# Performance work log

Hardware: AMD Instinct MI355X
Metric: run time of the kernel (lower is better)

Reference implementation:

```python
import jax, jax.numpy as jnp
import numpy as np

B, T, N, D = 8, 12, 325, 256
H = 8
HD = D // H
FF = 1024
SCALE = HD ** -0.5
EPS = 1e-5
NEG_INF = jnp.float32(-1e30)


def layernorm(x, w, b):
    mu = jnp.mean(x, axis=-1, keepdims=True)
    var = jnp.mean(jnp.square(x - mu), axis=-1, keepdims=True)
    return (x - mu) * jax.lax.rsqrt(var + EPS) * w + b


def mha(x, wq, bq, wk, bk, wv, bv, wo, bo, mask):
    # x: (G, L, D); mask: (L, L) bool, True = keep, or None
    G, L, _ = x.shape
    q = (x @ wq + bq).reshape(G, L, H, HD)
    k = (x @ wk + bk).reshape(G, L, H, HD)
    v = (x @ wv + bv).reshape(G, L, H, HD)
    scores = jnp.einsum('glhd,gmhd->ghlm', q, k) * SCALE
    if mask is not None:
        scores = jnp.where(mask[None, None], scores, NEG_INF)
    attn = jax.nn.softmax(scores, axis=-1)
    out = jnp.einsum('ghlm,gmhd->glhd', attn, v).reshape(G, L, D)
    return out @ wo + bo


def setup_inputs() -> dict:
    key = jax.random.key(0)
    ks = jax.random.split(key, 16)
    s = 0.02
    inp = {
        'x': jax.random.normal(ks[0], (B, T, N, D), jnp.float32),
        'adj_mask': jax.random.randint(ks[1], (N, N), 0, 2, jnp.int32),
        'sa_wq': jax.random.normal(ks[2], (D, D)) * s, 'sa_bq': jnp.zeros((D,)),
        'sa_wk': jax.random.normal(ks[3], (D, D)) * s, 'sa_bk': jnp.zeros((D,)),
        'sa_wv': jax.random.normal(ks[4], (D, D)) * s, 'sa_bv': jnp.zeros((D,)),
        'sa_wo': jax.random.normal(ks[5], (D, D)) * s, 'sa_bo': jnp.zeros((D,)),
        'sa_ln_w': jnp.ones((D,)), 'sa_ln_b': jnp.zeros((D,)),
        'ta_wq': jax.random.normal(ks[6], (D, D)) * s, 'ta_bq': jnp.zeros((D,)),
        'ta_wk': jax.random.normal(ks[7], (D, D)) * s, 'ta_bk': jnp.zeros((D,)),
        'ta_wv': jax.random.normal(ks[8], (D, D)) * s, 'ta_bv': jnp.zeros((D,)),
        'ta_wo': jax.random.normal(ks[9], (D, D)) * s, 'ta_bo': jnp.zeros((D,)),
        'ta_ln_w': jnp.ones((D,)), 'ta_ln_b': jnp.zeros((D,)),
        'f_w1': jax.random.normal(ks[10], (D, FF)) * s, 'f_b1': jnp.zeros((FF,)),
        'f_w2': jax.random.normal(ks[11], (FF, D)) * s, 'f_b2': jnp.zeros((D,)),
        'f_ln_w': jnp.ones((D,)), 'f_ln_b': jnp.zeros((D,)),
    }
    return inp


def reference(x, adj_mask,
              sa_wq, sa_bq, sa_wk, sa_bk, sa_wv, sa_bv, sa_wo, sa_bo, sa_ln_w, sa_ln_b,
              ta_wq, ta_bq, ta_wk, ta_bk, ta_wv, ta_bv, ta_wo, ta_bo, ta_ln_w, ta_ln_b,
              f_w1, f_b1, f_w2, f_b2, f_ln_w, f_ln_b):
    # Spatial attention over N at each (b, t)
    xs = x.reshape(B * T, N, D)
    sa = mha(xs, sa_wq, sa_bq, sa_wk, sa_bk, sa_wv, sa_bv, sa_wo, sa_bo,
             adj_mask != 0).reshape(B, T, N, D)
    x = layernorm(x + sa, sa_ln_w, sa_ln_b)

    # Temporal attention over T at each (b, n), causal
    xt = x.transpose(0, 2, 1, 3).reshape(B * N, T, D)
    causal = jnp.tril(jnp.ones((T, T), dtype=bool))
    ta = mha(xt, ta_wq, ta_bq, ta_wk, ta_bk, ta_wv, ta_bv, ta_wo, ta_bo, causal)
    ta = ta.reshape(B, N, T, D).transpose(0, 2, 1, 3)
    x = layernorm(x + ta, ta_ln_w, ta_ln_b)

    # FFN with exact GELU (torch nn.GELU default)
    h = jax.nn.gelu(x @ f_w1 + f_b1, approximate=False)
    out = layernorm(x + (h @ f_w2 + f_b2), f_ln_w, f_ln_b)
    return out
```

## Files before the change

kernel.cpp:

```cpp
#include <hip/hip_runtime.h>
#include <hip/hip_bf16.h>
#include <math.h>

#define B_   8
#define T_   12
#define NN   325
#define DD   256
#define HH   8
#define HD   32
#define FFD  1024
#define MTOK (B_*T_*NN)
#define QKVD 768
#define ATT_SCALE 0.17677669529663687f
#define LN_EPS 1e-5f
#define NEG_BIG (-1e30f)

typedef __attribute__((ext_vector_type(8))) __bf16 bf16x8;
typedef __attribute__((ext_vector_type(4))) float  f32x4;
typedef __attribute__((ext_vector_type(4))) short  shortx4;
typedef __attribute__((ext_vector_type(8))) unsigned short ushortx8;

static __device__ inline float bf2f(unsigned short u) {
  union { float f; unsigned int i; } c; c.i = ((unsigned int)u) << 16; return c.f;
}

#if __has_builtin(__builtin_amdgcn_mfma_f32_16x16x16bf16_1k)
#define MFMA16(a,b,c) __builtin_amdgcn_mfma_f32_16x16x16bf16_1k((a),(b),(c),0,0,0)
#else
static __device__ inline f32x4 mfma16_fn(shortx4 a, shortx4 b, f32x4 c) {
  f32x4 d;
  asm volatile("v_mfma_f32_16x16x16_bf16 %0, %1, %2, %3"
               : "=v"(d) : "v"(a), "v"(b), "v"(c));
  return d;
}
#define MFMA16(a,b,c) mfma16_fn((a),(b),(c))
#endif

#define GLDS(gsrc, ldst) \
  __builtin_amdgcn_global_load_lds((const __attribute__((address_space(1))) void*)(gsrc), \
                                   (__attribute__((address_space(3))) void*)(ldst), 16, 0, 0)

__global__ __launch_bounds__(256) void gemm_mfma(
    const __hip_bfloat16* __restrict__ A,
    const __hip_bfloat16* __restrict__ Wt,
    const float* __restrict__ bias,
    float* __restrict__ Cf, __hip_bfloat16* __restrict__ Cb,
    int Mr, int Nr, int Kr, int mode)
{
  __shared__ __hip_bfloat16 As[2][128 * 32];
  __shared__ __hip_bfloat16 Bs[2][128 * 32];

  const int NB  = Nr >> 7;
  const int nwg = gridDim.x;
  {
  }
  const int orig = blockIdx.x;
  const int qq = nwg >> 3, rr = nwg & 7;
  const int xcd = orig & 7, off = orig >> 3;
  const int id = (xcd < rr ? xcd * (qq + 1) : rr * (qq + 1) + (xcd - rr) * qq) + off;
  const int n0 = (id % NB) * 128;
  const int m0 = (id / NB) * 128;

  const int tid  = threadIdx.x;
  const int w    = tid >> 6;
  const int lane = tid & 63;
  const int wr   = w >> 1, wc = w & 1;

  f32x4 acc[4][4] = {};

  const int srow = w * 32 + (lane >> 2);
  const int scol = (lane & 3) * 8;
  int ar0 = m0 + srow;      if (ar0 >= Mr) ar0 = Mr - 1;
  int ar1 = m0 + srow + 16; if (ar1 >= Mr) ar1 = Mr - 1;
  const size_t aOff0 = (size_t)ar0 * Kr + scol;
  const size_t aOff1 = (size_t)ar1 * Kr + scol;
  const size_t bOff0 = (size_t)(n0 + srow) * Kr + scol;
  const size_t bOff1 = (size_t)(n0 + srow + 16) * Kr + scol;

  const int lr = lane & 15;
  const int kb = (lane >> 4) * 8;
  const int nk = Kr >> 5;

#define STAGE_T(buf, k0) do { \
    GLDS(&A[aOff0 + (k0)],  &As[buf][(w * 32) * 32]); \
    GLDS(&A[aOff1 + (k0)],  &As[buf][(w * 32 + 16) * 32]); \
    GLDS(&Wt[bOff0 + (k0)], &Bs[buf][(w * 32) * 32]); \
    GLDS(&Wt[bOff1 + (k0)], &Bs[buf][(w * 32 + 16) * 32]); \
  } while (0)

#define COMPUTE_T(buf) do { \
    bf16x8 af[4], bfr[4]; \
    _Pragma("unroll") for (int i = 0; i < 4; ++i) { \
      af[i]  = *(const bf16x8*)&As[buf][(wr * 64 + i * 16 + lr) * 32 + kb]; \
      bfr[i] = *(const bf16x8*)&Bs[buf][(wc * 64 + i * 16 + lr) * 32 + kb]; \
    } \
    _Pragma("unroll") for (int i = 0; i < 4; ++i) \
      _Pragma("unroll") for (int j = 0; j < 4; ++j) \
        acc[i][j] = __builtin_amdgcn_mfma_f32_16x16x32_bf16(af[i], bfr[j], acc[i][j], 0, 0, 0); \
  } while (0)

  STAGE_T(0, 0);
  __syncthreads();
  int cur = 0;
  for (int k = 1; k < nk; ++k) {
    STAGE_T(cur ^ 1, k * 32);
    COMPUTE_T(cur);
    __syncthreads();
    cur ^= 1;
  }
  COMPUTE_T(cur);
#undef STAGE_T
#undef COMPUTE_T

  const int rg = lane >> 4;
  #pragma unroll
  for (int i = 0; i < 4; ++i) {
    int rowb = m0 + wr * 64 + i * 16 + rg * 4;
    #pragma unroll
    for (int j = 0; j < 4; ++j) {
      int col = n0 + wc * 64 + j * 16 + lr;
      float bv = bias[col];
      #pragma unroll
      for (int q = 0; q < 4; ++q) {
        int gm = rowb + q;
        if (gm >= Mr) continue;
        float c = acc[i][j][q] + bv;
        if (mode == 0) {
          Cf[(size_t)gm * Nr + col] = c;
        } else {
          if (mode == 1) c = 0.5f * c * (1.f + erff(c * 0.70710678118654752f));
          Cb[(size_t)gm * Nr + col] = __float2bfloat16(c);
        }
      }
    }
  }
}

__global__ __launch_bounds__(256) void wt_cvt(
    const float* __restrict__ W, __hip_bfloat16* __restrict__ Wt, int K, int N)
{
  __shared__ float t[32][33];
  const int n0 = blockIdx.x * 32, k0 = blockIdx.y * 32;
  const int tx = threadIdx.x & 31, ty = threadIdx.x >> 5;
  #pragma unroll
  for (int i = 0; i < 32; i += 8)
    t[ty + i][tx] = W[(size_t)(k0 + ty + i) * N + n0 + tx];
  __syncthreads();
  #pragma unroll
  for (int i = 0; i < 32; i += 8)
    Wt[(size_t)(n0 + ty + i) * K + k0 + tx] = __float2bfloat16(t[tx][ty + i]);
}

__global__ __launch_bounds__(256) void cvt_bf16(
    const float* __restrict__ x, __hip_bfloat16* __restrict__ y, int n4)
{
  int i = blockIdx.x * 256 + threadIdx.x;
  if (i >= n4) return;
  float4 v = reinterpret_cast<const float4*>(x)[i];
  union { shortx4 s; __hip_bfloat16 h[4]; } u;
  u.h[0] = __float2bfloat16(v.x); u.h[1] = __float2bfloat16(v.y);
  u.h[2] = __float2bfloat16(v.z); u.h[3] = __float2bfloat16(v.w);
  reinterpret_cast<shortx4*>(y)[i] = u.s;
}

__global__ __launch_bounds__(256) void bias_cat3(
    const float* __restrict__ a, const float* __restrict__ b,
    const float* __restrict__ c, float* __restrict__ o)
{
  int i = blockIdx.x * 256 + threadIdx.x;
  if (i < 256) o[i] = a[i];
  else if (i < 512) o[i] = b[i - 256];
  else if (i < 768) o[i] = c[i - 512];
}

__global__ __launch_bounds__(256) void maskpack(
    const int* __restrict__ adj, unsigned int* __restrict__ mb)
{
  int idx = blockIdx.x * 256 + threadIdx.x;
  if (idx >= NN * 11) return;
  int l = idx / 11, w = idx % 11;
  unsigned int bits = 0;
  #pragma unroll 4
  for (int b = 0; b < 32; ++b) {
    int m = w * 32 + b;
    if (m < NN && adj[l * NN + m] != 0) bits |= (1u << b);
  }
  mb[idx] = bits;
}

__global__ __launch_bounds__(256) void spatial_attn_mfma(
    const __hip_bfloat16* __restrict__ qkv,
    const unsigned int* __restrict__ mb,
    __hip_bfloat16* __restrict__ out)
{
  constexpr int KP = 40;
  constexpr int VP = 340;
  __shared__ unsigned short Kl[336 * KP];
  __shared__ unsigned short Vt[32 * VP];

  const int g = blockIdx.x, h = blockIdx.y;
  const int tid = threadIdx.x;
  const int w = tid >> 6, lane = tid & 63;
  const int lq = lane & 15, lg = lane >> 4;

  const size_t baseQ = (size_t)g * NN * QKVD + (size_t)h * HD;
  const size_t baseK = baseQ + 256;
  const size_t baseV = baseQ + 512;

  for (int idx = tid; idx < 32 * (VP - NN); idx += 256) {
    int d = idx / (VP - NN), kk = NN + idx % (VP - NN);
    Vt[d * VP + kk] = 0;
  }
  for (int idx = tid; idx < NN * 4; idx += 256) {
    int row = idx >> 2, cc = (idx & 3) * 8;
    union { bf16x8 v; unsigned short u[8]; } kv, vv;
    kv.v = *(const bf16x8*)&qkv[baseK + (size_t)row * QKVD + cc];
    *(bf16x8*)&Kl[row * KP + cc] = kv.v;
    vv.v = *(const bf16x8*)&qkv[baseV + (size_t)row * QKVD + cc];
    #pragma unroll
    for (int j = 0; j < 8; ++j) Vt[(cc + j) * VP + row] = vv.u[j];
  }
  __syncthreads();

  for (int qt = w; qt < 21; qt += 4) {
    const int query = qt * 16 + lq;
    const int qc = query < NN ? query : NN - 1;
    const bf16x8 qf = *(const bf16x8*)&qkv[baseQ + (size_t)qc * QKVD + lg * 8];
    const unsigned int* mrow = &mb[qc * 11];

    f32x4 accL = {0.f, 0.f, 0.f, 0.f};
    f32x4 accH = {0.f, 0.f, 0.f, 0.f};
    float mrun = -INFINITY, lrun = 0.f;

    for (int t = 0; t < 21; ++t) {
      bf16x8 kf = *(const bf16x8*)&Kl[(t * 16 + lq) * KP + lg * 8];
      f32x4 st = __builtin_amdgcn_mfma_f32_16x16x32_bf16(
          kf, qf, (f32x4){0.f, 0.f, 0.f, 0.f}, 0, 0, 0);
      const unsigned int mw = mrow[t >> 1];
      const int kbase = t * 16 + lg * 4;
      const int bbase = (t & 1) * 16 + lg * 4;
      float s[4];
      #pragma unroll
      for (int q = 0; q < 4; ++q) {
        float fill = (kbase + q < NN) ? NEG_BIG : -INFINITY;
        s[q] = ((mw >> (bbase + q)) & 1u) ? st[q] * ATT_SCALE : fill;
      }
      float tmax = fmaxf(fmaxf(s[0], s[1]), fmaxf(s[2], s[3]));
      tmax = fmaxf(tmax, __shfl_xor(tmax, 16));
      tmax = fmaxf(tmax, __shfl_xor(tmax, 32));
      const float mnew = fmaxf(mrun, tmax);
      const float corr = __expf(mrun - mnew);
      float p0 = __expf(s[0] - mnew), p1 = __expf(s[1] - mnew);
      float p2 = __expf(s[2] - mnew), p3 = __expf(s[3] - mnew);
      float ps = p0 + p1 + p2 + p3;
      ps += __shfl_xor(ps, 16);
      ps += __shfl_xor(ps, 32);
      lrun = lrun * corr + ps;
      mrun = mnew;
      accL *= corr; accH *= corr;
      union { shortx4 s4; __hip_bfloat16 hh[4]; } up;
      up.hh[0] = __float2bfloat16(p0); up.hh[1] = __float2bfloat16(p1);
      up.hh[2] = __float2bfloat16(p2); up.hh[3] = __float2bfloat16(p3);
      shortx4 vaL = *(const shortx4*)&Vt[lq * VP + kbase];
      shortx4 vaH = *(const shortx4*)&Vt[(lq + 16) * VP + kbase];
      accL = MFMA16(vaL, up.s4, accL);
      accH = MFMA16(vaH, up.s4, accH);
    }

    if (query < NN) {
      const float inv = 1.f / lrun;
      const size_t ob = ((size_t)(g * NN + query)) * DD + (size_t)h * HD;
      union { shortx4 s4; __hip_bfloat16 hh[4]; } uL, uH;
      #pragma unroll
      for (int q = 0; q < 4; ++q) {
        uL.hh[q] = __float2bfloat16(accL[q] * inv);
        uH.hh[q] = __float2bfloat16(accH[q] * inv);
      }
      *(shortx4*)&out[ob + lg * 4]      = uL.s4;
      *(shortx4*)&out[ob + 16 + lg * 4] = uH.s4;
    }
  }
}

__global__ __launch_bounds__(256) void temporal_attn(
    const __hip_bfloat16* __restrict__ qkv, __hip_bfloat16* __restrict__ out)
{
  int idx = blockIdx.x * 256 + threadIdx.x;
  const int total = B_ * NN * HH * T_;
  if (idx >= total) return;

  int t  = idx % T_;
  int h  = (idx / T_) % HH;
  int n  = (idx / (T_ * HH)) % NN;
  int b  = idx / (T_ * HH * NN);

  const size_t tq = (size_t)((b * T_ + t) * NN + n) * QKVD + h * HD;
  float qr[HD];
  #pragma unroll
  for (int c8 = 0; c8 < 4; ++c8) {
    ushortx8 u = *(const ushortx8*)&qkv[tq + c8 * 8];
    #pragma unroll
    for (int j = 0; j < 8; ++j) qr[c8 * 8 + j] = bf2f(u[j]);
  }

  float o[HD] = {};
  float mrun = -INFINITY, lrun = 0.f;

  for (int tt = 0; tt <= t; ++tt) {
    const size_t tk = (size_t)((b * T_ + tt) * NN + n) * QKVD + h * HD;
    float s = 0.f;
    #pragma unroll
    for (int c8 = 0; c8 < 4; ++c8) {
      ushortx8 u = *(const ushortx8*)&qkv[tk + 256 + c8 * 8];
      #pragma unroll
      for (int j = 0; j < 8; ++j) s += qr[c8 * 8 + j] * bf2f(u[j]);
    }
    s *= ATT_SCALE;

    float mnew = fmaxf(mrun, s);
    float corr = __expf(mrun - mnew);
    float p = __expf(s - mnew);
    lrun = lrun * corr + p;
    #pragma unroll
    for (int c8 = 0; c8 < 4; ++c8) {
      ushortx8 u = *(const ushortx8*)&qkv[tk + 512 + c8 * 8];
      #pragma unroll
      for (int j = 0; j < 8; ++j) o[c8 * 8 + j] = o[c8 * 8 + j] * corr + p * bf2f(u[j]);
    }
    mrun = mnew;
  }

  float inv = 1.f / lrun;
  __hip_bfloat16* op = out + ((size_t)((b * T_ + t) * NN + n)) * DD + h * HD;
  #pragma unroll
  for (int d0 = 0; d0 < HD; d0 += 4) {
    union { shortx4 s; __hip_bfloat16 h4[4]; } u;
    #pragma unroll
    for (int j = 0; j < 4; ++j) u.h4[j] = __float2bfloat16(o[d0 + j] * inv);
    *reinterpret_cast<shortx4*>(op + d0) = u.s;
  }
}

__global__ __launch_bounds__(64) void add_ln(
    const float* __restrict__ x, const float* __restrict__ r,
    const float* __restrict__ w, const float* __restrict__ bb,
    float* __restrict__ y, __hip_bfloat16* __restrict__ ybf)
{
  const size_t row = blockIdx.x;
  const int lane = threadIdx.x;

  const float4 xv = reinterpret_cast<const float4*>(x + row * DD)[lane];
  const float4 rv = reinterpret_cast<const float4*>(r + row * DD)[lane];
  float e[4] = {xv.x + rv.x, xv.y + rv.y, xv.z + rv.z, xv.w + rv.w};

  float s  = e[0] + e[1] + e[2] + e[3];
  float ss = e[0]*e[0] + e[1]*e[1] + e[2]*e[2] + e[3]*e[3];
  #pragma unroll
  for (int off = 32; off > 0; off >>= 1) {
    s  += __shfl_xor(s,  off, 64);
    ss += __shfl_xor(ss, off, 64);
  }
  float mu  = s * (1.f / DD);
  float var = ss * (1.f / DD) - mu * mu;
  float rs  = rsqrtf(var + LN_EPS);

  const float4 wv = reinterpret_cast<const float4*>(w)[lane];
  const float4 bv = reinterpret_cast<const float4*>(bb)[lane];
  float o0 = (e[0] - mu) * rs * wv.x + bv.x;
  float o1 = (e[1] - mu) * rs * wv.y + bv.y;
  float o2 = (e[2] - mu) * rs * wv.z + bv.z;
  float o3 = (e[3] - mu) * rs * wv.w + bv.w;
  float4 yv = {o0, o1, o2, o3};
  reinterpret_cast<float4*>(y + row * DD)[lane] = yv;
  if (ybf) {
    union { shortx4 s4; __hip_bfloat16 h4[4]; } u;
    u.h4[0] = __float2bfloat16(o0); u.h4[1] = __float2bfloat16(o1);
    u.h4[2] = __float2bfloat16(o2); u.h4[3] = __float2bfloat16(o3);
    reinterpret_cast<shortx4*>(ybf + row * DD)[lane] = u.s4;
  }
}

extern "C" void kernel_launch(void* const* d_in, const int* in_sizes, int n_in,
                              void* d_out, int out_size, void* d_ws, size_t ws_size,
                              hipStream_t stream)
{
  const float* x0   = (const float*)d_in[0];
  const int*   adj  = (const int*)  d_in[1];
  const float* sa_wq = (const float*)d_in[2];
  const float* sa_bq = (const float*)d_in[3];
  const float* sa_wk = (const float*)d_in[4];
  const float* sa_bk = (const float*)d_in[5];
  const float* sa_wv = (const float*)d_in[6];
  const float* sa_bv = (const float*)d_in[7];
  const float* sa_wo = (const float*)d_in[8];
  const float* sa_bo = (const float*)d_in[9];
  const float* sa_lw = (const float*)d_in[10];
  const float* sa_lb = (const float*)d_in[11];
  const float* ta_wq = (const float*)d_in[12];
  const float* ta_bq = (const float*)d_in[13];
  const float* ta_wk = (const float*)d_in[14];
  const float* ta_bk = (const float*)d_in[15];
  const float* ta_wv = (const float*)d_in[16];
  const float* ta_bv = (const float*)d_in[17];
  const float* ta_wo = (const float*)d_in[18];
  const float* ta_bo = (const float*)d_in[19];
  const float* ta_lw = (const float*)d_in[20];
  const float* ta_lb = (const float*)d_in[21];
  const float* f_w1  = (const float*)d_in[22];
  const float* f_b1  = (const float*)d_in[23];
  const float* f_w2  = (const float*)d_in[24];
  const float* f_b2  = (const float*)d_in[25];
  const float* f_lw  = (const float*)d_in[26];
  const float* f_lb  = (const float*)d_in[27];

  float* out = (float*)d_out;
  float* ws  = (float*)d_ws;

  const size_t P = (size_t)MTOK * DD;
  if (ws_size < 7 * P * sizeof(float)) return;

  float* R0 = ws;
  __hip_bfloat16* QKVb = (__hip_bfloat16*)(ws + P);
  __hip_bfloat16* HIDb = (__hip_bfloat16*)(ws + P);
  float* R3 = ws + 3 * P;
  float* R4 = ws + 4 * P;
  __hip_bfloat16* X0b  = (__hip_bfloat16*)(ws + 5 * P);
  __hip_bfloat16* X1b  = (__hip_bfloat16*)(ws + 5 * P + P / 2);
  __hip_bfloat16* ATTb = (__hip_bfloat16*)(ws + 6 * P);
  __hip_bfloat16* Wb   = (__hip_bfloat16*)(ws + 6 * P + P / 2);

  __hip_bfloat16* sa_qkv_t = Wb;
  __hip_bfloat16* ta_qkv_t = Wb + 196608;
  __hip_bfloat16* sa_wo_t  = Wb + 393216;
  __hip_bfloat16* ta_wo_t  = Wb + 458752;
  __hip_bfloat16* f_w1_t   = Wb + 524288;
  __hip_bfloat16* f_w2_t   = Wb + 786432;
  float* sa_qkvb = (float*)(Wb + 1048576);
  float* ta_qkvb = sa_qkvb + 768;
  unsigned int* MB = (unsigned int*)(ta_qkvb + 768);

  wt_cvt<<<dim3(DD/32, DD/32), 256, 0, stream>>>(sa_wq, sa_qkv_t,          DD, DD);
  wt_cvt<<<dim3(DD/32, DD/32), 256, 0, stream>>>(sa_wk, sa_qkv_t + 65536,  DD, DD);
  wt_cvt<<<dim3(DD/32, DD/32), 256, 0, stream>>>(sa_wv, sa_qkv_t + 131072, DD, DD);
  wt_cvt<<<dim3(DD/32, DD/32), 256, 0, stream>>>(ta_wq, ta_qkv_t,          DD, DD);
  wt_cvt<<<dim3(DD/32, DD/32), 256, 0, stream>>>(ta_wk, ta_qkv_t + 65536,  DD, DD);
  wt_cvt<<<dim3(DD/32, DD/32), 256, 0, stream>>>(ta_wv, ta_qkv_t + 131072, DD, DD);
  wt_cvt<<<dim3(DD/32, DD/32), 256, 0, stream>>>(sa_wo, sa_wo_t, DD, DD);
  wt_cvt<<<dim3(DD/32, DD/32), 256, 0, stream>>>(ta_wo, ta_wo_t, DD, DD);
  wt_cvt<<<dim3(FFD/32, DD/32), 256, 0, stream>>>(f_w1, f_w1_t, DD, FFD);
  wt_cvt<<<dim3(DD/32, FFD/32), 256, 0, stream>>>(f_w2, f_w2_t, FFD, DD);
  bias_cat3<<<3, 256, 0, stream>>>(sa_bq, sa_bk, sa_bv, sa_qkvb);
  bias_cat3<<<3, 256, 0, stream>>>(ta_bq, ta_bk, ta_bv, ta_qkvb);
  maskpack<<<(NN * 11 + 255) / 256, 256, 0, stream>>>(adj, MB);
  {
    int n4 = (int)(P / 4);
    cvt_bf16<<<(n4 + 255) / 256, 256, 0, stream>>>(x0, X0b, n4);
  }

  const int MBk = (MTOK + 127) / 128;
  auto gemm = [&](const __hip_bfloat16* A, const __hip_bfloat16* Wt, const float* bias,
                  float* Cf, __hip_bfloat16* Cb, int Nr, int Kr, int mode) {
    int nwg = (Nr / 128) * MBk;
    gemm_mfma<<<nwg, 256, 0, stream>>>(A, Wt, bias, Cf, Cb, MTOK, Nr, Kr, mode);
  };

  gemm(X0b, sa_qkv_t, sa_qkvb, nullptr, QKVb, QKVD, DD, 2);
  spatial_attn_mfma<<<dim3(B_ * T_, HH), 256, 0, stream>>>(QKVb, MB, ATTb);
  gemm(ATTb, sa_wo_t, sa_bo, R3, nullptr, DD, DD, 0);
  add_ln<<<MTOK, 64, 0, stream>>>(x0, R3, sa_lw, sa_lb, R4, X1b);

  gemm(X1b, ta_qkv_t, ta_qkvb, nullptr, QKVb, QKVD, DD, 2);
  {
    int total = B_ * NN * HH * T_;
    temporal_attn<<<(total + 255) / 256, 256, 0, stream>>>(QKVb, ATTb);
  }
  gemm(ATTb, ta_wo_t, ta_bo, R3, nullptr, DD, DD, 0);
  add_ln<<<MTOK, 64, 0, stream>>>(R4, R3, ta_lw, ta_lb, R0, X0b);

  gemm(X0b, f_w1_t, f_b1, nullptr, HIDb, FFD, DD, 1);
  gemm(HIDb, f_w2_t, f_b2, R3, nullptr, DD, FFD, 0);
  add_ln<<<MTOK, 64, 0, stream>>>(R0, R3, f_lw, f_lb, out, nullptr);
}
```

Measured before the change: 414.7 us.

## Swizzle GEMM LDS tiles and restructure double-buffer pipeline with explicit waitcnt

The GEMM's LDS layout gets an XOR-style column rotation on both the global-to-LDS staging and the fragment reads, to cut LDS bank conflicts. The main loop now prefetches two stages ahead. It uses explicit vmcnt/lgkmcnt waits and raw s_barrier in place of __syncthreads, so the next tile's global loads can be issued before the MFMAs run. This relies on hand-counted outstanding loads, so the count must match the four loads issued per stage. It also adds a second barrier per iteration.

Measured after the change: 413.2 us. Within noise of the previous version (-0.4%).

```diff
diff --git a/kernel.cpp b/kernel.cpp
--- a/kernel.cpp
+++ b/kernel.cpp
@@ -52,8 +52,6 @@
 
   const int NB  = Nr >> 7;
   const int nwg = gridDim.x;
-  {
-  }
   const int orig = blockIdx.x;
   const int qq = nwg >> 3, rr = nwg & 7;
   const int xcd = orig & 7, off = orig >> 3;
@@ -68,17 +66,27 @@
 
   f32x4 acc[4][4] = {};
 
-  const int srow = w * 32 + (lane >> 2);
-  const int scol = (lane & 3) * 8;
-  int ar0 = m0 + srow;      if (ar0 >= Mr) ar0 = Mr - 1;
-  int ar1 = m0 + srow + 16; if (ar1 >= Mr) ar1 = Mr - 1;
+  const int c4   = lane & 3;
+  const int r0   = w * 32 + (lane >> 2);
+  const int csw  = (c4 - (r0 >> 1)) & 3;
+  const int scol = csw * 8;
+  int ar0 = m0 + r0;      if (ar0 >= Mr) ar0 = Mr - 1;
+  int ar1 = m0 + r0 + 16; if (ar1 >= Mr) ar1 = Mr - 1;
   const size_t aOff0 = (size_t)ar0 * Kr + scol;
   const size_t aOff1 = (size_t)ar1 * Kr + scol;
-  const size_t bOff0 = (size_t)(n0 + srow) * Kr + scol;
-  const size_t bOff1 = (size_t)(n0 + srow + 16) * Kr + scol;
+  const size_t bOff0 = (size_t)(n0 + r0) * Kr + scol;
+  const size_t bOff1 = (size_t)(n0 + r0 + 16) * Kr + scol;
 
   const int lr = lane & 15;
-  const int kb = (lane >> 4) * 8;
+  const int lg = lane >> 4;
+  int offA[4], offB[4];
+  #pragma unroll
+  for (int i = 0; i < 4; ++i) {
+    int rA = wr * 64 + i * 16 + lr;
+    offA[i] = rA * 32 + (((lg + (rA >> 1)) & 3) * 8);
+    int rB = wc * 64 + i * 16 + lr;
+    offB[i] = rB * 32 + (((lg + (rB >> 1)) & 3) * 8);
+  }
   const int nk = Kr >> 5;
 
 #define STAGE_T(buf, k0) do { \
@@ -88,31 +96,36 @@
     GLDS(&Wt[bOff1 + (k0)], &Bs[buf][(w * 32 + 16) * 32]); \
   } while (0)
 
-#define COMPUTE_T(buf) do { \
-    bf16x8 af[4], bfr[4]; \
-    _Pragma("unroll") for (int i = 0; i < 4; ++i) { \
-      af[i]  = *(const bf16x8*)&As[buf][(wr * 64 + i * 16 + lr) * 32 + kb]; \
-      bfr[i] = *(const bf16x8*)&Bs[buf][(wc * 64 + i * 16 + lr) * 32 + kb]; \
-    } \
-    _Pragma("unroll") for (int i = 0; i < 4; ++i) \
-      _Pragma("unroll") for (int j = 0; j < 4; ++j) \
-        acc[i][j] = __builtin_amdgcn_mfma_f32_16x16x32_bf16(af[i], bfr[j], acc[i][j], 0, 0, 0); \
-  } while (0)
-
   STAGE_T(0, 0);
-  __syncthreads();
-  int cur = 0;
-  for (int k = 1; k < nk; ++k) {
-    STAGE_T(cur ^ 1, k * 32);
-    COMPUTE_T(cur);
-    __syncthreads();
-    cur ^= 1;
-  }
-  COMPUTE_T(cur);
+  if (nk > 1) STAGE_T(1, 32);
+
+  for (int k = 0; k < nk; ++k) {
+    if (k + 1 < nk) asm volatile("s_waitcnt vmcnt(4)" ::: "memory");
+    else            asm volatile("s_waitcnt vmcnt(0)" ::: "memory");
+    __builtin_amdgcn_s_barrier();
+
+    const int buf = k & 1;
+    bf16x8 af[4], bfr[4];
+    #pragma unroll
+    for (int i = 0; i < 4; ++i) {
+      af[i]  = *(const bf16x8*)&As[buf][offA[i]];
+      bfr[i] = *(const bf16x8*)&Bs[buf][offB[i]];
+    }
+    asm volatile("s_waitcnt lgkmcnt(0)" ::: "memory");
+    __builtin_amdgcn_sched_barrier(0);
+    __builtin_amdgcn_s_barrier();
+
+    if (k + 2 < nk) STAGE_T(buf, (k + 2) * 32);
+
+    #pragma unroll
+    for (int i = 0; i < 4; ++i)
+      #pragma unroll
+      for (int j = 0; j < 4; ++j)
+        acc[i][j] = __builtin_amdgcn_mfma_f32_16x16x32_bf16(af[i], bfr[j], acc[i][j], 0, 0, 0);
+  }
 #undef STAGE_T
-#undef COMPUTE_T
-
-  const int rg = lane >> 4;
+
+  const int rg = lg;
   #pragma unroll
   for (int i = 0; i < 4; ++i) {
     int rowb = m0 + wr * 64 + i * 16 + rg * 4;
```
